# Optimization experiments

Hardware: AMD Instinct MI355X
Metric: run time of the kernel (lower is better)

## Reference

```python
import jax, jax.numpy as jnp
import numpy as np

B, T, D = 4, 2048, 1024
GROUPS = 32
EPS = 1e-5
THETA = 10000.0


def _rope(x):
    # lucidrains RotaryEmbedding: interleaved pairs over the full dim
    d = x.shape[-1]
    t = x.shape[-2]
    inv_freq = 1.0 / (THETA ** (jnp.arange(0, d, 2, dtype=jnp.float32) / d))  # [d/2]
    freqs = jnp.arange(t, dtype=jnp.float32)[:, None] * inv_freq[None, :]      # [T, d/2]
    cos = jnp.cos(freqs).astype(x.dtype)
    sin = jnp.sin(freqs).astype(x.dtype)
    x1 = x[..., 0::2]
    x2 = x[..., 1::2]
    r1 = x1 * cos - x2 * sin
    r2 = x1 * sin + x2 * cos
    return jnp.stack([r1, r2], axis=-1).reshape(x.shape)


def _group_norm(z, weight, bias):
    # z: [N, C]; normalize per group of C//GROUPS channels
    n, c = z.shape
    zg = z.reshape(n, GROUPS, c // GROUPS)
    mean = zg.mean(axis=-1, keepdims=True)
    var = zg.var(axis=-1, keepdims=True)
    zg = (zg - mean) * jax.lax.rsqrt(var + EPS)
    return zg.reshape(n, c) * weight + bias


def setup_inputs() -> dict:
    key = jax.random.key(0)
    k1, k2, k3 = jax.random.split(key, 3)
    x = jax.random.normal(k1, (B, T, D), dtype=jnp.float32)
    W_in = jax.random.normal(k2, (D, 3 * D), dtype=jnp.float32) * (1.0 / np.sqrt(D))
    b_in = jax.random.normal(k3, (3 * D,), dtype=jnp.float32) * 0.02
    gn_weight = jnp.ones((D,), dtype=jnp.float32)
    gn_bias = jnp.zeros((D,), dtype=jnp.float32)
    return {"x": x, "W_in": W_in, "b_in": b_in, "gn_weight": gn_weight, "gn_bias": gn_bias}


def reference(x, W_in, b_in, gn_weight, gn_bias):
    b, t, c = x.shape
    qkv = x @ W_in + b_in                    # [B,T,3D]
    Q, K, V = jnp.split(qkv, 3, axis=-1)
    Q = jax.nn.relu(_rope(Q))
    K = jax.nn.relu(_rope(K))
    V = jax.nn.relu(V)
    A = jnp.einsum('btd,bsd->bts', Q, K)     # [B,T,T], no softmax
    y = jnp.einsum('bts,bsd->btd', A, V)     # [B,T,D]
    y = _group_norm(y.reshape(-1, c), gn_weight, gn_bias).reshape(b, t, c)
    # faithful to original: transpose(-2,-1).reshape(B,T,dim)
    return jnp.swapaxes(y, -2, -1).reshape(b, t, c)
```

## Files before the change

kernel.cpp:

```cpp
#include <hip/hip_runtime.h>


typedef unsigned short u16;
typedef __attribute__((ext_vector_type(8))) unsigned short u16x8;
typedef __attribute__((ext_vector_type(4))) float fx4;
typedef __attribute__((ext_vector_type(8))) __bf16 bfx8;

#define TP 129

__device__ __forceinline__ u16 f2bh(float v) {
  unsigned u = __float_as_uint(v);
  return (u16)((u + 0x7FFFu + ((u >> 16) & 1u)) >> 16);
}
__device__ __forceinline__ fx4 mfma16(bfx8 a, bfx8 b, fx4 c) {
  return __builtin_amdgcn_mfma_f32_16x16x32_bf16(a, b, c, 0, 0, 0);
}

__device__ __forceinline__ void gload16(const u16* g, u16* l) {
  __builtin_amdgcn_global_load_lds(
      (const __attribute__((address_space(1))) unsigned int*)(const void*)g,
      (__attribute__((address_space(3))) unsigned int*)(void*)l, 16, 0, 0);
}

__device__ __forceinline__ bfx8 ldsw(const u16* lds, int row, int slot) {
  const char* p = (const char*)lds + row * 128 + ((slot ^ (row & 7)) << 4);
  return __builtin_bit_cast(bfx8, *reinterpret_cast<const u16x8*>(p));
}

__device__ __forceinline__ void stage4(const u16* __restrict__ A,
                                       size_t rowBase, int stride, int k0,
                                       u16* lds, int w, int lane) {
#pragma unroll
  for (int i = 0; i < 4; ++i) {
    int c = ((w * 4 + i) << 6) + lane;
    int r = c >> 3, s = c & 7;
    int t = s ^ (r & 7);
    const u16* src = A + (rowBase + (size_t)r) * (size_t)stride + k0 + (t << 3);
    gload16(src, lds + ((w * 4 + i) << 9));
  }
}

__device__ inline void gemm_core_pipe(const u16* __restrict__ A, size_t aBase, int aStr,
                                      const u16* __restrict__ B, size_t bBase, int bStr, int K,
                                      u16* sA0, u16* sB0, u16* sA1, u16* sB1,
                                      fx4 acc[4][4], int w, int lane) {
  int wm = (w >> 1) * 64, wn = (w & 1) * 64;
  int lr = lane & 15, lk = lane >> 4;
  stage4(A, aBase, aStr, 0, sA0, w, lane);
  stage4(B, bBase, bStr, 0, sB0, w, lane);
  int NT = K >> 6;
  for (int t = 0; t < NT; ++t) {
    u16* cA = (t & 1) ? sA1 : sA0;
    u16* cB = (t & 1) ? sB1 : sB0;
    if (t + 1 < NT) {
      u16* nA = (t & 1) ? sA0 : sA1;
      u16* nB = (t & 1) ? sB0 : sB1;
      stage4(A, aBase, aStr, (t + 1) << 6, nA, w, lane);
      stage4(B, bBase, bStr, (t + 1) << 6, nB, w, lane);
      asm volatile("s_waitcnt vmcnt(8)" ::: "memory");
    } else {
      asm volatile("s_waitcnt vmcnt(0)" ::: "memory");
    }
    __builtin_amdgcn_s_barrier();
    __builtin_amdgcn_sched_barrier(0);
    bfx8 a[8], b[8];
#pragma unroll
    for (int h = 0; h < 2; ++h)
#pragma unroll
      for (int i = 0; i < 4; ++i) {
        a[h * 4 + i] = ldsw(cA, wm + i * 16 + lr, h * 4 + lk);
        b[h * 4 + i] = ldsw(cB, wn + i * 16 + lr, h * 4 + lk);
      }
    asm volatile("s_waitcnt lgkmcnt(0)" ::: "memory");
    __builtin_amdgcn_sched_barrier(0);
    __builtin_amdgcn_s_barrier();
#pragma unroll
    for (int h = 0; h < 2; ++h)
#pragma unroll
      for (int mi = 0; mi < 4; ++mi)
#pragma unroll
        for (int ni = 0; ni < 4; ++ni)
          acc[mi][ni] = mfma16(a[h * 4 + mi], b[h * 4 + ni], acc[mi][ni]);
  }
}

__global__ void k_prep(const float* __restrict__ x, const float* __restrict__ W,
                       u16* __restrict__ xh, u16* __restrict__ WTh,
                       float2* __restrict__ tabTI, float2* __restrict__ tabIT) {
  __shared__ float tile[32][33];
  int bid = blockIdx.x, tid = threadIdx.x;
  if (bid < 4096) {
    size_t i = ((size_t)bid * 256 + tid) * 8;
    fx4 v0 = *reinterpret_cast<const fx4*>(x + i);
    fx4 v1 = *reinterpret_cast<const fx4*>(x + i + 4);
    u16x8 h;
#pragma unroll
    for (int j = 0; j < 4; ++j) {
      h[j] = f2bh(v0[j]);
      h[4 + j] = f2bh(v1[j]);
    }
    *reinterpret_cast<u16x8*>(xh + i) = h;
  } else if (bid < 7168) {
    int idx = bid - 4096;
    int n0 = (idx % 96) * 32, k0 = (idx / 96) * 32;
    int c = tid & 31, r4 = tid >> 5;
#pragma unroll
    for (int it = 0; it < 4; ++it) {
      int r = r4 + it * 8;
      tile[r][c] = W[(size_t)(k0 + r) * 3072 + n0 + c];
    }
    __syncthreads();
#pragma unroll
    for (int it = 0; it < 4; ++it) {
      int r = r4 + it * 8;
      WTh[(size_t)(n0 + r) * 1024 + k0 + c] = f2bh(tile[c][r]);
    }
  } else {
    int half = (bid - 7168) >> 12;
    int idx = ((bid - 7168) & 4095) * 256 + tid;
    int t, i;
    if (half == 0) {
      t = idx >> 9;
      i = idx & 511;
    } else {
      i = idx >> 11;
      t = idx & 2047;
    }
    float invf = exp2f(-(float)i * (13.287712379549449f / 512.f));
    float ang = (float)t * invf, s, c;
    sincosf(ang, &s, &c);
    if (half == 0)
      tabTI[idx] = make_float2(c, s);
    else
      tabIT[idx] = make_float2(c, s);
  }
}

__global__ __launch_bounds__(256) void k_gemm1f(const u16* __restrict__ xh,
                                                const u16* __restrict__ WTh,
                                                const float* __restrict__ b_in,
                                                const float2* __restrict__ tabTI,
                                                const float2* __restrict__ tabIT,
                                                u16* __restrict__ Qh, u16* __restrict__ Kth,
                                                u16* __restrict__ Vth) {
  __shared__ __align__(16) float shbuf[128 * TP];
  u16* sA0 = (u16*)shbuf;
  u16* sB0 = sA0 + 128 * 64;
  u16* sA1 = sB0 + 128 * 64;
  u16* sB1 = sA1 + 128 * 64;
  int bid = blockIdx.x;
  int xcd = bid & 7, idx = bid >> 3;
  int mt = (xcd << 3) + (idx & 7), nt = idx >> 3;
  int m0 = mt << 7, n0 = nt << 7;
  int tid = threadIdx.x, lane = tid & 63, w = tid >> 6;
  int wm = (w >> 1) * 64, wn = (w & 1) * 64;
  int lr = lane & 15, lk = lane >> 4;
  fx4 acc[4][4];
#pragma unroll
  for (int i = 0; i < 4; ++i)
#pragma unroll
    for (int j = 0; j < 4; ++j) acc[i][j] = fx4{0.f, 0.f, 0.f, 0.f};

  gemm_core_pipe(xh, (size_t)m0, 1024, WTh, (size_t)n0, 1024, 1024,
                 sA0, sB0, sA1, sB1, acc, w, lane);

  float bv[4];
#pragma unroll
  for (int ni = 0; ni < 4; ++ni) bv[ni] = b_in[n0 + wn + ni * 16 + lr];
  __syncthreads();
#pragma unroll
  for (int mi = 0; mi < 4; ++mi)
#pragma unroll
    for (int ni = 0; ni < 4; ++ni)
#pragma unroll
      for (int r = 0; r < 4; ++r)
        shbuf[(wn + ni * 16 + lr) * TP + wm + mi * 16 + lk * 4 + r] = acc[mi][ni][r] + bv[ni];
  __syncthreads();

  int part = n0 >> 10;
  int d0 = n0 - (part << 10);
  int bb = m0 >> 11, tb = m0 & 2047;
  int rl0 = tid >> 4;
  int cc = (tid & 15) * 8;

  if (part == 2) {
#pragma unroll
    for (int pass = 0; pass < 8; ++pass) {
      int rl = rl0 + pass * 16;
      u16x8 o;
#pragma unroll
      for (int j = 0; j < 8; ++j) o[j] = f2bh(fmaxf(shbuf[rl * TP + cc + j], 0.f));
      *reinterpret_cast<u16x8*>(Vth + (((size_t)(bb << 10) + d0 + rl) << 11) + tb + cc) = o;
    }
  } else if (part == 1) {
#pragma unroll
    for (int pass = 0; pass < 8; ++pass) {
      int rl = rl0 + pass * 16;
      int d = d0 + rl;
      const float2* tp = tabIT + ((size_t)(d >> 1) << 11) + tb + cc;
      const float* e = shbuf + (rl & ~1) * TP + cc;
      const float* oo = shbuf + (rl | 1) * TP + cc;
      int isOdd = d & 1;
      u16x8 o;
#pragma unroll
      for (int j = 0; j < 8; ++j) {
        float2 cs = tp[j];
        float x1 = e[j], x2 = oo[j];
        float v = isOdd ? (x1 * cs.y + x2 * cs.x) : (x1 * cs.x - x2 * cs.y);
        o[j] = f2bh(fmaxf(v, 0.f));
      }
      *reinterpret_cast<u16x8*>(Kth + (((size_t)(bb << 10) + d) << 11) + tb + cc) = o;
    }
  } else {
#pragma unroll
    for (int pass = 0; pass < 8; ++pass) {
      int rl = rl0 + pass * 16;
      int m = m0 + rl, t = m & 2047;
      const float2* tp = tabTI + ((size_t)t << 9) + ((d0 + cc) >> 1);
      u16x8 o;
#pragma unroll
      for (int jp = 0; jp < 4; ++jp) {
        float x1 = shbuf[(cc + 2 * jp) * TP + rl];
        float x2 = shbuf[(cc + 2 * jp + 1) * TP + rl];
        float2 cs = tp[jp];
        o[2 * jp] = f2bh(fmaxf(x1 * cs.x - x2 * cs.y, 0.f));
        o[2 * jp + 1] = f2bh(fmaxf(x1 * cs.y + x2 * cs.x, 0.f));
      }
      *reinterpret_cast<u16x8*>(Qh + ((size_t)m << 10) + d0 + cc) = o;
    }
  }
}

__global__ __launch_bounds__(256) void k_gemm2(const u16* __restrict__ Kth, const u16* __restrict__ Vth,
                                               u16* __restrict__ KtVTh) {
  __shared__ u16 smem[4 * 128 * 64];
  u16* sA0 = smem;
  u16* sB0 = sA0 + 128 * 64;
  u16* sA1 = sB0 + 128 * 64;
  u16* sB1 = sA1 + 128 * 64;
  fx4 acc[4][4];
#pragma unroll
  for (int i = 0; i < 4; ++i)
#pragma unroll
    for (int j = 0; j < 4; ++j) acc[i][j] = fx4{0.f, 0.f, 0.f, 0.f};
  int bid = blockIdx.x;
  int xcd = bid & 7, idx = bid >> 3;
  int b = xcd >> 1;
  int mt = (xcd & 1) * 4 + (idx & 3), nt = idx >> 2;
  int m0 = mt << 7, n0 = nt << 7;
  int tid = threadIdx.x, lane = tid & 63, w = tid >> 6;
  const u16* Ab = Kth + ((size_t)b << 21);
  const u16* Bb = Vth + ((size_t)b << 21);
  gemm_core_pipe(Ab, (size_t)m0, 2048, Bb, (size_t)n0, 2048, 2048,
                 sA0, sB0, sA1, sB1, acc, w, lane);
  int wm = (w >> 1) * 64, wn = (w & 1) * 64, lr = lane & 15, lk = lane >> 4;
#pragma unroll
  for (int mi = 0; mi < 4; ++mi)
#pragma unroll
    for (int ni = 0; ni < 4; ++ni)
#pragma unroll
      for (int r = 0; r < 4; ++r) {
        int m = m0 + wm + mi * 16 + lk * 4 + r;
        int n = n0 + wn + ni * 16 + lr;
        KtVTh[((size_t)b << 20) + ((size_t)n << 10) + m] = f2bh(acc[mi][ni][r]);
      }
}

__global__ __launch_bounds__(256) void k_gemm3g(const u16* __restrict__ Qh, const u16* __restrict__ KtVTh,
                                                const float* __restrict__ gw, const float* __restrict__ gb,
                                                float* __restrict__ out) {
  __shared__ u16 smem[4 * 128 * 64];
  u16* sA0 = smem;
  u16* sB0 = sA0 + 128 * 64;
  u16* sA1 = sB0 + 128 * 64;
  u16* sB1 = sA1 + 128 * 64;
  fx4 acc[4][4];
#pragma unroll
  for (int i = 0; i < 4; ++i)
#pragma unroll
    for (int j = 0; j < 4; ++j) acc[i][j] = fx4{0.f, 0.f, 0.f, 0.f};
  int bid = blockIdx.x;
  int xcd = bid & 7, idx = bid >> 3;
  int b = xcd >> 1;
  int mt = (xcd & 1) * 8 + (idx & 7), nt = idx >> 3;
  int m0 = mt << 7, n0 = nt << 7;
  int tid = threadIdx.x, lane = tid & 63, w = tid >> 6;
  gemm_core_pipe(Qh, (size_t)(b * 2048 + m0), 1024, KtVTh + ((size_t)b << 20), (size_t)n0, 1024,
                 1024, sA0, sB0, sA1, sB1, acc, w, lane);
  int wm = (w >> 1) * 64, wn = (w & 1) * 64, lr = lane & 15, lk = lane >> 4;
  float wv[4], bvv[4];
#pragma unroll
  for (int ni = 0; ni < 4; ++ni) {
    int n = n0 + wn + ni * 16 + lr;
    wv[ni] = gw[n];
    bvv[ni] = gb[n];
  }
#pragma unroll
  for (int mi = 0; mi < 4; ++mi) {
    fx4 o0, o1, o2, o3;
#pragma unroll
    for (int r = 0; r < 4; ++r) {
      float v0 = acc[mi][0][r], v1 = acc[mi][1][r], v2 = acc[mi][2][r], v3 = acc[mi][3][r];
      float sA2 = v0 + v1, sB2 = v2 + v3;
#pragma unroll
      for (int mk = 1; mk <= 8; mk <<= 1) {
        sA2 += __shfl_xor(sA2, mk);
        sB2 += __shfl_xor(sB2, mk);
      }
      float mA = sA2 * (1.f / 32.f), mB = sB2 * (1.f / 32.f);
      float dA = (v0 - mA) * (v0 - mA) + (v1 - mA) * (v1 - mA);
      float dB = (v2 - mB) * (v2 - mB) + (v3 - mB) * (v3 - mB);
#pragma unroll
      for (int mk = 1; mk <= 8; mk <<= 1) {
        dA += __shfl_xor(dA, mk);
        dB += __shfl_xor(dB, mk);
      }
      float rA = rsqrtf(dA * (1.f / 32.f) + 1e-5f);
      float rB = rsqrtf(dB * (1.f / 32.f) + 1e-5f);
      o0[r] = (v0 - mA) * rA * wv[0] + bvv[0];
      o1[r] = (v1 - mA) * rA * wv[1] + bvv[1];
      o2[r] = (v2 - mB) * rB * wv[2] + bvv[2];
      o3[r] = (v3 - mB) * rB * wv[3] + bvv[3];
    }
    int mbase = m0 + wm + mi * 16 + lk * 4;
#pragma unroll
    for (int ni = 0; ni < 4; ++ni) {
      int n = n0 + wn + ni * 16 + lr;
      fx4 ov = (ni == 0) ? o0 : (ni == 1) ? o1 : (ni == 2) ? o2 : o3;
      *reinterpret_cast<fx4*>(out + (((size_t)(b << 10) + n) << 11) + mbase) = ov;
    }
  }
}

extern "C" void kernel_launch(void* const* d_in, const int* in_sizes, int n_in,
                              void* d_out, int out_size, void* d_ws, size_t ws_size,
                              hipStream_t stream) {
  const float* x = (const float*)d_in[0];
  const float* W = (const float*)d_in[1];
  const float* b_in = (const float*)d_in[2];
  const float* gnw = (const float*)d_in[3];
  const float* gnb = (const float*)d_in[4];
  float* out = (float*)d_out;
  char* ws = (char*)d_ws;

  u16* xh = (u16*)(ws + 0);
  u16* WTh = (u16*)(ws + 16777216);
  u16* Qh = (u16*)(ws + 23068672);
  u16* Kth = (u16*)(ws + 39845888);
  u16* Vth = (u16*)(ws + 56623104);
  u16* KtVTh = (u16*)(ws + 73400320);
  float2* tabTI = (float2*)(ws + 81788928);
  float2* tabIT = (float2*)(ws + 90177536);

  k_prep<<<15360, 256, 0, stream>>>(x, W, xh, WTh, tabTI, tabIT);
  k_gemm1f<<<1536, 256, 0, stream>>>(xh, WTh, b_in, tabTI, tabIT, Qh, Kth, Vth);
  k_gemm2<<<256, 256, 0, stream>>>(Kth, Vth, KtVTh);
  k_gemm3g<<<512, 256, 0, stream>>>(Qh, KtVTh, gnw, gnb, out);
}
```

Baseline: 140.3 us.

## Halve GEMM K-tile to 32 and split gemm1 epilogue staging into halves

```diff
diff --git a/kernel.cpp b/kernel.cpp
--- a/kernel.cpp
+++ b/kernel.cpp
@@ -6,7 +6,7 @@
 typedef __attribute__((ext_vector_type(4))) float fx4;
 typedef __attribute__((ext_vector_type(8))) __bf16 bfx8;
 
-#define TP 129
+#define TP 65
 
 __device__ __forceinline__ u16 f2bh(float v) {
   unsigned u = __float_as_uint(v);
@@ -22,21 +22,24 @@
       (__attribute__((address_space(3))) unsigned int*)(void*)l, 16, 0, 0);
 }
 
-__device__ __forceinline__ bfx8 ldsw(const u16* lds, int row, int slot) {
-  const char* p = (const char*)lds + row * 128 + ((slot ^ (row & 7)) << 4);
+__device__ __forceinline__ bfx8 ldsw32(const u16* lds, int row, int lk) {
+  int sr = row >> 1;
+  int t = ((row & 1) << 2) + lk;
+  const char* p = (const char*)lds + sr * 128 + ((t ^ (sr & 7)) << 4);
   return __builtin_bit_cast(bfx8, *reinterpret_cast<const u16x8*>(p));
 }
 
-__device__ __forceinline__ void stage4(const u16* __restrict__ A,
+__device__ __forceinline__ void stage2(const u16* __restrict__ A,
                                        size_t rowBase, int stride, int k0,
                                        u16* lds, int w, int lane) {
 #pragma unroll
-  for (int i = 0; i < 4; ++i) {
-    int c = ((w * 4 + i) << 6) + lane;
-    int r = c >> 3, s = c & 7;
-    int t = s ^ (r & 7);
-    const u16* src = A + (rowBase + (size_t)r) * (size_t)stride + k0 + (t << 3);
-    gload16(src, lds + ((w * 4 + i) << 9));
+  for (int i = 0; i < 2; ++i) {
+    int c = ((w * 2 + i) << 6) + lane;
+    int sr = c >> 3, s = c & 7;
+    int t = s ^ (sr & 7);
+    int row = 2 * sr + (t >> 2);
+    const u16* src = A + (rowBase + (size_t)row) * (size_t)stride + k0 + ((t & 3) << 3);
+    gload16(src, lds + ((w * 2 + i) << 9));
   }
 }
 
@@ -46,41 +49,37 @@
                                       fx4 acc[4][4], int w, int lane) {
   int wm = (w >> 1) * 64, wn = (w & 1) * 64;
   int lr = lane & 15, lk = lane >> 4;
-  stage4(A, aBase, aStr, 0, sA0, w, lane);
-  stage4(B, bBase, bStr, 0, sB0, w, lane);
-  int NT = K >> 6;
+  stage2(A, aBase, aStr, 0, sA0, w, lane);
+  stage2(B, bBase, bStr, 0, sB0, w, lane);
+  int NT = K >> 5;
   for (int t = 0; t < NT; ++t) {
     u16* cA = (t & 1) ? sA1 : sA0;
     u16* cB = (t & 1) ? sB1 : sB0;
     if (t + 1 < NT) {
       u16* nA = (t & 1) ? sA0 : sA1;
       u16* nB = (t & 1) ? sB0 : sB1;
-      stage4(A, aBase, aStr, (t + 1) << 6, nA, w, lane);
-      stage4(B, bBase, bStr, (t + 1) << 6, nB, w, lane);
-      asm volatile("s_waitcnt vmcnt(8)" ::: "memory");
+      stage2(A, aBase, aStr, (t + 1) << 5, nA, w, lane);
+      stage2(B, bBase, bStr, (t + 1) << 5, nB, w, lane);
+      asm volatile("s_waitcnt vmcnt(4)" ::: "memory");
     } else {
       asm volatile("s_waitcnt vmcnt(0)" ::: "memory");
     }
     __builtin_amdgcn_s_barrier();
     __builtin_amdgcn_sched_barrier(0);
-    bfx8 a[8], b[8];
-#pragma unroll
-    for (int h = 0; h < 2; ++h)
-#pragma unroll
-      for (int i = 0; i < 4; ++i) {
-        a[h * 4 + i] = ldsw(cA, wm + i * 16 + lr, h * 4 + lk);
-        b[h * 4 + i] = ldsw(cB, wn + i * 16 + lr, h * 4 + lk);
-      }
+    bfx8 a[4], b[4];
+#pragma unroll
+    for (int i = 0; i < 4; ++i) {
+      a[i] = ldsw32(cA, wm + i * 16 + lr, lk);
+      b[i] = ldsw32(cB, wn + i * 16 + lr, lk);
+    }
     asm volatile("s_waitcnt lgkmcnt(0)" ::: "memory");
     __builtin_amdgcn_sched_barrier(0);
     __builtin_amdgcn_s_barrier();
 #pragma unroll
-    for (int h = 0; h < 2; ++h)
-#pragma unroll
-      for (int mi = 0; mi < 4; ++mi)
-#pragma unroll
-        for (int ni = 0; ni < 4; ++ni)
-          acc[mi][ni] = mfma16(a[h * 4 + mi], b[h * 4 + ni], acc[mi][ni]);
+    for (int mi = 0; mi < 4; ++mi)
+#pragma unroll
+      for (int ni = 0; ni < 4; ++ni)
+        acc[mi][ni] = mfma16(a[mi], b[ni], acc[mi][ni]);
   }
 }
 
@@ -145,9 +144,9 @@
                                                 u16* __restrict__ Vth) {
   __shared__ __align__(16) float shbuf[128 * TP];
   u16* sA0 = (u16*)shbuf;
-  u16* sB0 = sA0 + 128 * 64;
-  u16* sA1 = sB0 + 128 * 64;
-  u16* sB1 = sA1 + 128 * 64;
+  u16* sB0 = sA0 + 64 * 64;
+  u16* sA1 = sB0 + 64 * 64;
+  u16* sB1 = sA1 + 64 * 64;
   int bid = blockIdx.x;
   int xcd = bid & 7, idx = bid >> 3;
   int mt = (xcd << 3) + (idx & 7), nt = idx >> 3;
@@ -164,80 +163,89 @@
   gemm_core_pipe(xh, (size_t)m0, 1024, WTh, (size_t)n0, 1024, 1024,
                  sA0, sB0, sA1, sB1, acc, w, lane);
 
-  float bv[4];
-#pragma unroll
-  for (int ni = 0; ni < 4; ++ni) bv[ni] = b_in[n0 + wn + ni * 16 + lr];
-  __syncthreads();
-#pragma unroll
-  for (int mi = 0; mi < 4; ++mi)
-#pragma unroll
-    for (int ni = 0; ni < 4; ++ni)
-#pragma unroll
-      for (int r = 0; r < 4; ++r)
-        shbuf[(wn + ni * 16 + lr) * TP + wm + mi * 16 + lk * 4 + r] = acc[mi][ni][r] + bv[ni];
-  __syncthreads();
-
   int part = n0 >> 10;
   int d0 = n0 - (part << 10);
-  int bb = m0 >> 11, tb = m0 & 2047;
-  int rl0 = tid >> 4;
-  int cc = (tid & 15) * 8;
-
-  if (part == 2) {
-#pragma unroll
-    for (int pass = 0; pass < 8; ++pass) {
-      int rl = rl0 + pass * 16;
-      u16x8 o;
-#pragma unroll
-      for (int j = 0; j < 8; ++j) o[j] = f2bh(fmaxf(shbuf[rl * TP + cc + j], 0.f));
-      *reinterpret_cast<u16x8*>(Vth + (((size_t)(bb << 10) + d0 + rl) << 11) + tb + cc) = o;
-    }
-  } else if (part == 1) {
-#pragma unroll
-    for (int pass = 0; pass < 8; ++pass) {
-      int rl = rl0 + pass * 16;
-      int d = d0 + rl;
-      const float2* tp = tabIT + ((size_t)(d >> 1) << 11) + tb + cc;
-      const float* e = shbuf + (rl & ~1) * TP + cc;
-      const float* oo = shbuf + (rl | 1) * TP + cc;
-      int isOdd = d & 1;
-      u16x8 o;
-#pragma unroll
-      for (int j = 0; j < 8; ++j) {
-        float2 cs = tp[j];
-        float x1 = e[j], x2 = oo[j];
-        float v = isOdd ? (x1 * cs.y + x2 * cs.x) : (x1 * cs.x - x2 * cs.y);
-        o[j] = f2bh(fmaxf(v, 0.f));
-      }
-      *reinterpret_cast<u16x8*>(Kth + (((size_t)(bb << 10) + d) << 11) + tb + cc) = o;
-    }
-  } else {
-#pragma unroll
-    for (int pass = 0; pass < 8; ++pass) {
-      int rl = rl0 + pass * 16;
-      int m = m0 + rl, t = m & 2047;
-      const float2* tp = tabTI + ((size_t)t << 9) + ((d0 + cc) >> 1);
-      u16x8 o;
-#pragma unroll
-      for (int jp = 0; jp < 4; ++jp) {
-        float x1 = shbuf[(cc + 2 * jp) * TP + rl];
-        float x2 = shbuf[(cc + 2 * jp + 1) * TP + rl];
-        float2 cs = tp[jp];
-        o[2 * jp] = f2bh(fmaxf(x1 * cs.x - x2 * cs.y, 0.f));
-        o[2 * jp + 1] = f2bh(fmaxf(x1 * cs.y + x2 * cs.x, 0.f));
-      }
-      *reinterpret_cast<u16x8*>(Qh + ((size_t)m << 10) + d0 + cc) = o;
+  int bb = m0 >> 11, tbase = m0 & 2047;
+  float bv[4];
+#pragma unroll
+  for (int ni = 0; ni < 4; ++ni) bv[ni] = b_in[n0 + wn + ni * 16 + lr];
+
+#pragma unroll
+  for (int h = 0; h < 2; ++h) {
+    __syncthreads();
+    if ((w >> 1) == h) {
+#pragma unroll
+      for (int mi = 0; mi < 4; ++mi)
+#pragma unroll
+        for (int ni = 0; ni < 4; ++ni)
+#pragma unroll
+          for (int r = 0; r < 4; ++r) {
+            int ml = mi * 16 + lk * 4 + r;
+            int nl = wn + ni * 16 + lr;
+            shbuf[nl * TP + ml] = acc[mi][ni][r] + bv[ni];
+          }
+    }
+    __syncthreads();
+    int tb = tbase + h * 64;
+    if (part == 2) {
+#pragma unroll
+      for (int pass = 0; pass < 4; ++pass) {
+        int item = pass * 256 + tid;
+        int nl = item >> 3, c8 = (item & 7) * 8;
+        u16x8 o;
+#pragma unroll
+        for (int j = 0; j < 8; ++j) o[j] = f2bh(fmaxf(shbuf[nl * TP + c8 + j], 0.f));
+        *reinterpret_cast<u16x8*>(Vth + (((size_t)(bb << 10) + d0 + nl) << 11) + tb + c8) = o;
+      }
+    } else if (part == 1) {
+#pragma unroll
+      for (int pass = 0; pass < 4; ++pass) {
+        int item = pass * 256 + tid;
+        int nl = item >> 3, c8 = (item & 7) * 8;
+        int d = d0 + nl;
+        const float2* tp = tabIT + ((size_t)(d >> 1) << 11) + tb + c8;
+        const float* e = shbuf + (nl & ~1) * TP + c8;
+        const float* oo = shbuf + (nl | 1) * TP + c8;
+        int isOdd = d & 1;
+        u16x8 o;
+#pragma unroll
+        for (int j = 0; j < 8; ++j) {
+          float2 cs = tp[j];
+          float x1 = e[j], x2 = oo[j];
+          float v = isOdd ? (x1 * cs.y + x2 * cs.x) : (x1 * cs.x - x2 * cs.y);
+          o[j] = f2bh(fmaxf(v, 0.f));
+        }
+        *reinterpret_cast<u16x8*>(Kth + (((size_t)(bb << 10) + d) << 11) + tb + c8) = o;
+      }
+    } else {
+#pragma unroll
+      for (int pass = 0; pass < 4; ++pass) {
+        int item = pass * 256 + tid;
+        int ml = item >> 4, c16 = (item & 15) * 8;
+        int m = m0 + h * 64 + ml, t = m & 2047;
+        const float2* tp = tabTI + ((size_t)t << 9) + ((d0 + c16) >> 1);
+        u16x8 o;
+#pragma unroll
+        for (int jp = 0; jp < 4; ++jp) {
+          float x1 = shbuf[(c16 + 2 * jp) * TP + ml];
+          float x2 = shbuf[(c16 + 2 * jp + 1) * TP + ml];
+          float2 cs = tp[jp];
+          o[2 * jp] = f2bh(fmaxf(x1 * cs.x - x2 * cs.y, 0.f));
+          o[2 * jp + 1] = f2bh(fmaxf(x1 * cs.y + x2 * cs.x, 0.f));
+        }
+        *reinterpret_cast<u16x8*>(Qh + ((size_t)m << 10) + d0 + c16) = o;
+      }
     }
   }
 }
 
 __global__ __launch_bounds__(256) void k_gemm2(const u16* __restrict__ Kth, const u16* __restrict__ Vth,
                                                u16* __restrict__ KtVTh) {
-  __shared__ u16 smem[4 * 128 * 64];
+  __shared__ u16 smem[4 * 64 * 64];
   u16* sA0 = smem;
-  u16* sB0 = sA0 + 128 * 64;
-  u16* sA1 = sB0 + 128 * 64;
-  u16* sB1 = sA1 + 128 * 64;
+  u16* sB0 = sA0 + 64 * 64;
+  u16* sA1 = sB0 + 64 * 64;
+  u16* sB1 = sA1 + 64 * 64;
   fx4 acc[4][4];
 #pragma unroll
   for (int i = 0; i < 4; ++i)
@@ -269,11 +277,11 @@
 __global__ __launch_bounds__(256) void k_gemm3g(const u16* __restrict__ Qh, const u16* __restrict__ KtVTh,
                                                 const float* __restrict__ gw, const float* __restrict__ gb,
                                                 float* __restrict__ out) {
-  __shared__ u16 smem[4 * 128 * 64];
+  __shared__ u16 smem[4 * 64 * 64];
   u16* sA0 = smem;
-  u16* sB0 = sA0 + 128 * 64;
-  u16* sA1 = sB0 + 128 * 64;
-  u16* sB1 = sA1 + 128 * 64;
+  u16* sB0 = sA0 + 64 * 64;
+  u16* sA1 = sB0 + 64 * 64;
+  u16* sB1 = sA1 + 64 * 64;
   fx4 acc[4][4];
 #pragma unroll
   for (int i = 0; i < 4; ++i)
```

New measurement: 164.8 us. 17.5% more time.

## Fuse x fp32-to-bf16 conversion into QKV GEMM loads; halve gemm2 M-tile

Applied to the files above, without the earlier changes.

```diff
diff --git a/kernel.cpp b/kernel.cpp
--- a/kernel.cpp
+++ b/kernel.cpp
@@ -37,6 +37,19 @@
     int t = s ^ (r & 7);
     const u16* src = A + (rowBase + (size_t)r) * (size_t)stride + k0 + (t << 3);
     gload16(src, lds + ((w * 4 + i) << 9));
+  }
+}
+
+__device__ __forceinline__ void stageA2(const u16* __restrict__ A,
+                                        size_t rowBase, int stride, int k0,
+                                        u16* lds, int w, int lane) {
+#pragma unroll
+  for (int i = 0; i < 2; ++i) {
+    int c = ((w * 2 + i) << 6) + lane;
+    int r = c >> 3, s = c & 7;
+    int t = s ^ (r & 7);
+    const u16* src = A + (rowBase + (size_t)r) * (size_t)stride + k0 + (t << 3);
+    gload16(src, lds + ((w * 2 + i) << 9));
   }
 }
 
@@ -84,24 +97,12 @@
   }
 }
 
-__global__ void k_prep(const float* __restrict__ x, const float* __restrict__ W,
-                       u16* __restrict__ xh, u16* __restrict__ WTh,
+__global__ void k_prep(const float* __restrict__ W, u16* __restrict__ WTh,
                        float2* __restrict__ tabTI, float2* __restrict__ tabIT) {
   __shared__ float tile[32][33];
   int bid = blockIdx.x, tid = threadIdx.x;
-  if (bid < 4096) {
-    size_t i = ((size_t)bid * 256 + tid) * 8;
-    fx4 v0 = *reinterpret_cast<const fx4*>(x + i);
-    fx4 v1 = *reinterpret_cast<const fx4*>(x + i + 4);
-    u16x8 h;
-#pragma unroll
-    for (int j = 0; j < 4; ++j) {
-      h[j] = f2bh(v0[j]);
-      h[4 + j] = f2bh(v1[j]);
-    }
-    *reinterpret_cast<u16x8*>(xh + i) = h;
-  } else if (bid < 7168) {
-    int idx = bid - 4096;
+  if (bid < 3072) {
+    int idx = bid;
     int n0 = (idx % 96) * 32, k0 = (idx / 96) * 32;
     int c = tid & 31, r4 = tid >> 5;
 #pragma unroll
@@ -116,8 +117,8 @@
       WTh[(size_t)(n0 + r) * 1024 + k0 + c] = f2bh(tile[c][r]);
     }
   } else {
-    int half = (bid - 7168) >> 12;
-    int idx = ((bid - 7168) & 4095) * 256 + tid;
+    int half = (bid - 3072) >> 12;
+    int idx = ((bid - 3072) & 4095) * 256 + tid;
     int t, i;
     if (half == 0) {
       t = idx >> 9;
@@ -136,7 +137,7 @@
   }
 }
 
-__global__ __launch_bounds__(256) void k_gemm1f(const u16* __restrict__ xh,
+__global__ __launch_bounds__(256) void k_gemm1f(const float* __restrict__ x32,
                                                 const u16* __restrict__ WTh,
                                                 const float* __restrict__ b_in,
                                                 const float2* __restrict__ tabTI,
@@ -161,8 +162,88 @@
 #pragma unroll
     for (int j = 0; j < 4; ++j) acc[i][j] = fx4{0.f, 0.f, 0.f, 0.f};
 
-  gemm_core_pipe(xh, (size_t)m0, 1024, WTh, (size_t)n0, 1024, 1024,
-                 sA0, sB0, sA1, sB1, acc, w, lane);
+  int acr[4], act[4];
+#pragma unroll
+  for (int i = 0; i < 4; ++i) {
+    int c = ((w * 4 + i) << 6) + lane;
+    acr[i] = c >> 3;
+    act[i] = (c & 7) ^ (acr[i] & 7);
+  }
+  fx4 av[8];
+
+#pragma unroll
+  for (int i = 0; i < 4; ++i) {
+    const float* src = x32 + (size_t)(m0 + acr[i]) * 1024 + (act[i] << 3);
+    av[i * 2] = *reinterpret_cast<const fx4*>(src);
+    av[i * 2 + 1] = *reinterpret_cast<const fx4*>(src + 4);
+  }
+  stage4(WTh, (size_t)n0, 1024, 0, sB0, w, lane);
+#pragma unroll
+  for (int i = 0; i < 4; ++i) {
+    int c = ((w * 4 + i) << 6) + lane;
+    u16x8 hh;
+#pragma unroll
+    for (int j = 0; j < 4; ++j) {
+      hh[j] = f2bh(av[i * 2][j]);
+      hh[4 + j] = f2bh(av[i * 2 + 1][j]);
+    }
+    *reinterpret_cast<u16x8*>(sA0 + (size_t)c * 8) = hh;
+  }
+
+  const int NT = 16;
+  for (int t = 0; t < NT; ++t) {
+    u16* cA = (t & 1) ? sA1 : sA0;
+    u16* cB = (t & 1) ? sB1 : sB0;
+    if (t + 1 < NT) {
+      u16* nB = (t & 1) ? sB0 : sB1;
+      int k0 = (t + 1) << 6;
+#pragma unroll
+      for (int i = 0; i < 4; ++i) {
+        const float* src = x32 + (size_t)(m0 + acr[i]) * 1024 + k0 + (act[i] << 3);
+        av[i * 2] = *reinterpret_cast<const fx4*>(src);
+        av[i * 2 + 1] = *reinterpret_cast<const fx4*>(src + 4);
+      }
+      stage4(WTh, (size_t)n0, 1024, k0, nB, w, lane);
+      asm volatile("s_waitcnt vmcnt(12)" ::: "memory");
+    } else {
+      asm volatile("s_waitcnt vmcnt(0)" ::: "memory");
+    }
+    asm volatile("s_waitcnt lgkmcnt(0)" ::: "memory");
+    __builtin_amdgcn_s_barrier();
+    __builtin_amdgcn_sched_barrier(0);
+    bfx8 a[8], b[8];
+#pragma unroll
+    for (int h = 0; h < 2; ++h)
+#pragma unroll
+      for (int i = 0; i < 4; ++i) {
+        a[h * 4 + i] = ldsw(cA, wm + i * 16 + lr, h * 4 + lk);
+        b[h * 4 + i] = ldsw(cB, wn + i * 16 + lr, h * 4 + lk);
+      }
+    asm volatile("s_waitcnt lgkmcnt(0)" ::: "memory");
+    __builtin_amdgcn_sched_barrier(0);
+    __builtin_amdgcn_s_barrier();
+#pragma unroll
+    for (int h = 0; h < 2; ++h)
+#pragma unroll
+      for (int mi = 0; mi < 4; ++mi)
+#pragma unroll
+        for (int ni = 0; ni < 4; ++ni)
+          acc[mi][ni] = mfma16(a[h * 4 + mi], b[h * 4 + ni], acc[mi][ni]);
+    if (t + 1 < NT) {
+      u16* nA = (t & 1) ? sA0 : sA1;
+#pragma unroll
+      for (int i = 0; i < 4; ++i) {
+        int c = ((w * 4 + i) << 6) + lane;
+        u16x8 hh;
+#pragma unroll
+        for (int j = 0; j < 4; ++j) {
+          hh[j] = f2bh(av[i * 2][j]);
+          hh[4 + j] = f2bh(av[i * 2 + 1][j]);
+        }
+        *reinterpret_cast<u16x8*>(nA + (size_t)c * 8) = hh;
+      }
+    }
+  }
 
   float bv[4];
 #pragma unroll
@@ -233,35 +314,71 @@
 
 __global__ __launch_bounds__(256) void k_gemm2(const u16* __restrict__ Kth, const u16* __restrict__ Vth,
                                                u16* __restrict__ KtVTh) {
-  __shared__ u16 smem[4 * 128 * 64];
+  __shared__ u16 smem[2 * (64 + 128) * 64];
   u16* sA0 = smem;
-  u16* sB0 = sA0 + 128 * 64;
+  u16* sB0 = sA0 + 64 * 64;
   u16* sA1 = sB0 + 128 * 64;
-  u16* sB1 = sA1 + 128 * 64;
-  fx4 acc[4][4];
+  u16* sB1 = sA1 + 64 * 64;
+  fx4 acc[4][2];
 #pragma unroll
   for (int i = 0; i < 4; ++i)
 #pragma unroll
-    for (int j = 0; j < 4; ++j) acc[i][j] = fx4{0.f, 0.f, 0.f, 0.f};
+    for (int j = 0; j < 2; ++j) acc[i][j] = fx4{0.f, 0.f, 0.f, 0.f};
   int bid = blockIdx.x;
   int xcd = bid & 7, idx = bid >> 3;
   int b = xcd >> 1;
-  int mt = (xcd & 1) * 4 + (idx & 3), nt = idx >> 2;
-  int m0 = mt << 7, n0 = nt << 7;
+  int mt = (xcd & 1) * 8 + (idx & 7), nt = idx >> 3;
+  int m0 = mt << 6, n0 = nt << 7;
   int tid = threadIdx.x, lane = tid & 63, w = tid >> 6;
+  int wn2 = w * 32;
+  int lr = lane & 15, lk = lane >> 4;
   const u16* Ab = Kth + ((size_t)b << 21);
   const u16* Bb = Vth + ((size_t)b << 21);
-  gemm_core_pipe(Ab, (size_t)m0, 2048, Bb, (size_t)n0, 2048, 2048,
-                 sA0, sB0, sA1, sB1, acc, w, lane);
-  int wm = (w >> 1) * 64, wn = (w & 1) * 64, lr = lane & 15, lk = lane >> 4;
+
+  stageA2(Ab, (size_t)m0, 2048, 0, sA0, w, lane);
+  stage4(Bb, (size_t)n0, 2048, 0, sB0, w, lane);
+  const int NT = 32;
+  for (int t = 0; t < NT; ++t) {
+    u16* cA = (t & 1) ? sA1 : sA0;
+    u16* cB = (t & 1) ? sB1 : sB0;
+    if (t + 1 < NT) {
+      u16* nA = (t & 1) ? sA0 : sA1;
+      u16* nB = (t & 1) ? sB0 : sB1;
+      stageA2(Ab, (size_t)m0, 2048, (t + 1) << 6, nA, w, lane);
+      stage4(Bb, (size_t)n0, 2048, (t + 1) << 6, nB, w, lane);
+      asm volatile("s_waitcnt vmcnt(6)" ::: "memory");
+    } else {
+      asm volatile("s_waitcnt vmcnt(0)" ::: "memory");
+    }
+    __builtin_amdgcn_s_barrier();
+    __builtin_amdgcn_sched_barrier(0);
+    bfx8 a[8], bfr[4];
+#pragma unroll
+    for (int h = 0; h < 2; ++h) {
+#pragma unroll
+      for (int i = 0; i < 4; ++i) a[h * 4 + i] = ldsw(cA, i * 16 + lr, h * 4 + lk);
+#pragma unroll
+      for (int j = 0; j < 2; ++j) bfr[h * 2 + j] = ldsw(cB, wn2 + j * 16 + lr, h * 4 + lk);
+    }
+    asm volatile("s_waitcnt lgkmcnt(0)" ::: "memory");
+    __builtin_amdgcn_sched_barrier(0);
+    __builtin_amdgcn_s_barrier();
+#pragma unroll
+    for (int h = 0; h < 2; ++h)
+#pragma unroll
+      for (int mi = 0; mi < 4; ++mi)
+#pragma unroll
+        for (int ni = 0; ni < 2; ++ni)
+          acc[mi][ni] = mfma16(a[h * 4 + mi], bfr[h * 2 + ni], acc[mi][ni]);
+  }
 #pragma unroll
   for (int mi = 0; mi < 4; ++mi)
 #pragma unroll
-    for (int ni = 0; ni < 4; ++ni)
+    for (int ni = 0; ni < 2; ++ni)
 #pragma unroll
       for (int r = 0; r < 4; ++r) {
-        int m = m0 + wm + mi * 16 + lk * 4 + r;
-        int n = n0 + wn + ni * 16 + lr;
+        int m = m0 + mi * 16 + lk * 4 + r;
+        int n = n0 + wn2 + ni * 16 + lr;
         KtVTh[((size_t)b << 20) + ((size_t)n << 10) + m] = f2bh(acc[mi][ni][r]);
       }
 }
@@ -343,7 +460,6 @@
   float* out = (float*)d_out;
   char* ws = (char*)d_ws;
 
-  u16* xh = (u16*)(ws + 0);
   u16* WTh = (u16*)(ws + 16777216);
   u16* Qh = (u16*)(ws + 23068672);
   u16* Kth = (u16*)(ws + 39845888);
@@ -352,8 +468,8 @@
   float2* tabTI = (float2*)(ws + 81788928);
   float2* tabIT = (float2*)(ws + 90177536);
 
-  k_prep<<<15360, 256, 0, stream>>>(x, W, xh, WTh, tabTI, tabIT);
-  k_gemm1f<<<1536, 256, 0, stream>>>(xh, WTh, b_in, tabTI, tabIT, Qh, Kth, Vth);
-  k_gemm2<<<256, 256, 0, stream>>>(Kth, Vth, KtVTh);
+  k_prep<<<11264, 256, 0, stream>>>(W, WTh, tabTI, tabIT);
+  k_gemm1f<<<1536, 256, 0, stream>>>(x, WTh, b_in, tabTI, tabIT, Qh, Kth, Vth);
+  k_gemm2<<<512, 256, 0, stream>>>(Kth, Vth, KtVTh);
   k_gemm3g<<<512, 256, 0, stream>>>(Qh, KtVTh, gnw, gnb, out);
 }
```

Measured after the change: 147.9 us. 5.4% more time.
